# Performance work log

Hardware: AMD Instinct MI355X
Metric: run time of the kernel (lower is better)

## Reference

```python
import jax, jax.numpy as jnp
import numpy as np
from jax import lax

PAD, EOS, SOS = 0, 1, 2
B, S, V, NT, E, H = 64, 256, 50000, 64, 300, 500  # H = hidden per direction (HIDDEN_SIZE//2)


def setup_inputs():
    key = jax.random.key(0)
    ks = jax.random.split(key, 24)
    x = jax.random.randint(ks[0], (B, S), 1, V)          # no PAD tokens -> mask all ones
    y0 = jax.random.randint(ks[1], (B, S), 3, NT)        # gold tags, avoid special tags
    embed = jax.random.normal(ks[2], (V, E)) * 0.1
    embed = embed.at[PAD].set(0.0)                       # padding_idx=PAD
    inp = {"x": x, "y0": y0, "embed": embed}
    ki = 3
    for l, din in enumerate([E, 2 * H]):                 # layer0 in=E, layer1 in=2H
        for d in ("f", "b"):
            inp[f"w_ih_l{l}{d}"] = jax.random.normal(ks[ki], (4 * H, din)) * 0.05; ki += 1
            inp[f"w_hh_l{l}{d}"] = jax.random.normal(ks[ki], (4 * H, H)) * 0.05; ki += 1
            inp[f"b_l{l}{d}"] = jnp.zeros((4 * H,))       # b_ih + b_hh combined
    inp["W_out"] = jax.random.normal(ks[ki], (NT, 2 * H)) * 0.05; ki += 1
    inp["b_out"] = jnp.zeros((NT,))
    trans = jax.random.normal(ks[ki], (NT, NT))
    trans = trans.at[SOS, :].set(-10000.0).at[:, EOS].set(-10000.0)
    trans = trans.at[:, PAD].set(-10000.0).at[PAD, :].set(-10000.0)
    trans = trans.at[PAD, EOS].set(0.0).at[PAD, PAD].set(0.0)
    inp["trans"] = trans
    return inp


def _lstm_dir(xs, w_ih, w_hh, b, reverse):
    # xs: [B,S,D] -> outputs [B,S,H]; PyTorch gate order i,f,g,o
    def step(carry, x_t):
        h, c = carry
        g = x_t @ w_ih.T + h @ w_hh.T + b
        i, f, gg, o = jnp.split(g, 4, axis=-1)
        c = jax.nn.sigmoid(f) * c + jax.nn.sigmoid(i) * jnp.tanh(gg)
        h = jax.nn.sigmoid(o) * jnp.tanh(c)
        return (h, c), h
    bz = xs.shape[0]
    init = (jnp.zeros((bz, H), xs.dtype), jnp.zeros((bz, H), xs.dtype))
    _, hs = lax.scan(step, init, jnp.swapaxes(xs, 0, 1), reverse=reverse)
    return jnp.swapaxes(hs, 0, 1)


def _forward(x, y0, embed, w_ih_l0f, w_hh_l0f, b_l0f, w_ih_l0b, w_hh_l0b, b_l0b,
             w_ih_l1f, w_hh_l1f, b_l1f, w_ih_l1b, w_hh_l1b, b_l1b, W_out, b_out, trans):
    h0 = embed[x]                                        # [B,S,E]
    h1 = jnp.concatenate([_lstm_dir(h0, w_ih_l0f, w_hh_l0f, b_l0f, False),
                          _lstm_dir(h0, w_ih_l0b, w_hh_l0b, b_l0b, True)], -1)
    h2 = jnp.concatenate([_lstm_dir(h1, w_ih_l1f, w_hh_l1f, b_l1f, False),
                          _lstm_dir(h1, w_ih_l1b, w_hh_l1b, b_l1b, True)], -1)
    mask = (x > 0).astype(h2.dtype)                      # [B,S]
    emit = (h2 @ W_out.T + b_out) * mask[..., None]      # [B,S,NT]
    # --- CRF partition function Z (batched logsumexp DP) ---
    score0 = jnp.full((B, NT), -10000.0, emit.dtype).at[:, SOS].set(0.0)
    def step(score, inp):
        e_t, m_t = inp                                   # [B,NT], [B]
        # new[b,i] = lse_j(score[b,j] + trans[i,j] + e_t[b,i])
        z = score[:, None, :] + trans[None, :, :] + e_t[:, :, None]
        new = jax.nn.logsumexp(z, axis=-1)
        return jnp.where(m_t[:, None] > 0, new, score), None
    scoreZ, _ = lax.scan(step, score0, (jnp.swapaxes(emit, 0, 1), jnp.swapaxes(mask, 0, 1)))
    Z = jax.nn.logsumexp(scoreZ, axis=-1)                # [B]
    # --- gold path score ---
    yext = jnp.concatenate([jnp.full((B, 1), SOS, dtype=y0.dtype), y0], 1)  # [B,S+1]
    e_gold = jnp.take_along_axis(emit, yext[:, 1:, None], axis=-1)[..., 0]   # [B,S]
    t_gold = trans[yext[:, 1:], yext[:, :-1]] * mask                         # [B,S]
    gold = jnp.sum(e_gold + t_gold, axis=1)
    return Z - gold                                      # [B] NLL per sample


def reference(x, y0, embed, w_ih_l0f, w_hh_l0f, b_l0f, w_ih_l0b, w_hh_l0b, b_l0b,
              w_ih_l1f, w_hh_l1f, b_l1f, w_ih_l1b, w_hh_l1b, b_l1b, W_out, b_out, trans):
    return _forward(x, y0, embed, w_ih_l0f, w_hh_l0f, b_l0f, w_ih_l0b, w_hh_l0b, b_l0b,
                    w_ih_l1f, w_hh_l1f, b_l1f, w_ih_l1b, w_hh_l1b, b_l1b, W_out, b_out, trans)
```

## Files before the change

### kernel.cpp

```cpp
#include <hip/hip_runtime.h>
#include <hip/hip_bf16.h>
#include <cstdint>

#define B_ 64
#define S_ 256
#define V_ 50000
#define NT_ 64
#define E_ 300
#define H_ 500
#define SOS_ 2

typedef __hip_bfloat16 bf16;
typedef unsigned short ushort_t;
typedef __attribute__((ext_vector_type(8))) __bf16 v8bf;
typedef __attribute__((ext_vector_type(4))) float f32x4;
typedef __attribute__((ext_vector_type(4))) unsigned int u32x4;

__device__ __forceinline__ float sigm(float x) { return 1.f / (1.f + __expf(-x)); }
__device__ __forceinline__ float tanh_fast(float x) {
    float xx = fminf(fmaxf(x, -15.f), 15.f);
    float e = __expf(2.f * xx);
    return (e - 1.f) / (e + 1.f);
}

__device__ __forceinline__ float bfu_to_f(ushort_t u) {
    unsigned int v = ((unsigned int)u) << 16;
    return __builtin_bit_cast(float, v);
}
__device__ __forceinline__ ushort_t f_to_bfu(float f) {
    return __builtin_bit_cast(ushort_t, __float2bfloat16(f));
}

__device__ __forceinline__ void store_val(float* p, float v) { *p = v; }
__device__ __forceinline__ void store_val(ushort_t* p, float v) { *p = f_to_bfu(v); }

__device__ __forceinline__ v8bf load16_coh(const ushort_t* p) {
    v8bf r;
    asm volatile("global_load_dwordx4 %0, %1, off sc0 sc1" : "=v"(r) : "v"(p) : "memory");
    return r;
}
__device__ __forceinline__ void store8_coh(ushort_t* p, uint2 v) {
    asm volatile("global_store_dwordx2 %0, %1, off sc0 sc1" :: "v"(p), "v"(v) : "memory");
}

__global__ void dbg_kernel(float* out, float v) {
    if (threadIdx.x < 64) out[threadIdx.x] = v;
}

__global__ void gather_kernel(const int* __restrict__ x, const float* __restrict__ embed,
                              ushort_t* __restrict__ h0) {
    int m = blockIdx.x;
    int tok = x[m];
    const float* src = embed + (size_t)tok * E_;
    ushort_t* dst = h0 + (size_t)m * 320;
    for (int e = threadIdx.x; e < 320; e += blockDim.x)
        dst[e] = (e < E_) ? f_to_bfu(src[e]) : (ushort_t)0;
}

__global__ void conv_w_kernel(const float* __restrict__ in, ushort_t* __restrict__ out,
                              int N, int Kout, int Kin, int split, int real) {
    int idx = blockIdx.x * 256 + threadIdx.x;
    if (idx >= N * Kout) return;
    int n = idx / Kout, k = idx % Kout;
    int half = (k >= split) ? 1 : 0;
    int ki = k - half * split;
    float v = (ki < real) ? in[(size_t)n * Kin + half * real + ki] : 0.f;
    out[idx] = f_to_bfu(v);
}

template <bool HS>
__device__ __forceinline__ float loadA(const ushort_t* A, int m, int k, int K) {
    size_t idx;
    if (HS) {
        int dir = (k >= H_) ? 1 : 0;
        idx = (((size_t)dir * B_ + (m >> 8)) * S_ + (m & 255)) * 512 + (k - dir * H_);
    } else {
        idx = (size_t)m * K + k;
    }
    return bfu_to_f(A[idx]);
}

template <bool HS, typename OutT>
__global__ __launch_bounds__(256) void gemm_nt(const ushort_t* __restrict__ A,
                                               const float* __restrict__ W0,
                                               const float* __restrict__ b0,
                                               OutT* __restrict__ C0,
                                               int M, int N, int K) {
    const float* W = W0;
    const float* bias = b0;
    OutT* C = C0;
    const int n0 = blockIdx.y * 64;
    const int tid = threadIdx.x;
    const int tx = tid & 15, ty = tid >> 4;

    __shared__ float As[16][68];
    __shared__ float Bs[16][68];

    float acc[4][4] = {};

    for (int k0 = 0; k0 < K; k0 += 16) {
        for (int e = tid; e < 1024; e += 256) {
            int r = e >> 4, kk = e & 15;
            int k = k0 + kk;
            int m = blockIdx.x * 64 + r;
            As[kk][r] = (k < K) ? loadA<HS>(A, m, k, K) : 0.f;
            int n = n0 + r;
            Bs[kk][r] = (k < K && n < N) ? W[(size_t)n * K + k] : 0.f;
        }
        __syncthreads();
#pragma unroll
        for (int kk = 0; kk < 16; ++kk) {
            float4 a = *(const float4*)&As[kk][ty << 2];
            float4 w = *(const float4*)&Bs[kk][tx << 2];
            acc[0][0] += a.x * w.x; acc[0][1] += a.x * w.y; acc[0][2] += a.x * w.z; acc[0][3] += a.x * w.w;
            acc[1][0] += a.y * w.x; acc[1][1] += a.y * w.y; acc[1][2] += a.y * w.z; acc[1][3] += a.y * w.w;
            acc[2][0] += a.z * w.x; acc[2][1] += a.z * w.y; acc[2][2] += a.z * w.z; acc[2][3] += a.z * w.w;
            acc[3][0] += a.w * w.x; acc[3][1] += a.w * w.y; acc[3][2] += a.w * w.z; acc[3][3] += a.w * w.w;
        }
        __syncthreads();
    }

#pragma unroll
    for (int i = 0; i < 4; ++i) {
        int r = (ty << 2) + i;
        int m = blockIdx.x * 64 + r;
#pragma unroll
        for (int j = 0; j < 4; ++j) {
            int n = n0 + (tx << 2) + j;
            if (n < N) store_val(&C[(size_t)m * N + n], acc[i][j] + bias[n]);
        }
    }
}

template <int AV>
__global__ __launch_bounds__(256) void gemm_mfma(const ushort_t* __restrict__ A,
                                                 const ushort_t* __restrict__ Wf,
                                                 const ushort_t* __restrict__ Wb,
                                                 const float* __restrict__ bf_,
                                                 const float* __restrict__ bb_,
                                                 ushort_t* __restrict__ Cf,
                                                 ushort_t* __restrict__ Cb,
                                                 int Nn, int Kp) {
    const ushort_t* W = blockIdx.z ? Wb : Wf;
    const float* bias = blockIdx.z ? bb_ : bf_;
    ushort_t* C = blockIdx.z ? Cb : Cf;
    const int t = blockIdx.x;
    const int n0 = blockIdx.y * 64;
    const int tid = threadIdx.x;
    const int lane = tid & 63;
    const int wv = tid >> 6;
    const int wn = wv & 1, wb = wv >> 1;
    const int l15 = lane & 15, kgrp = lane >> 4;

    __shared__ ushort_t wlds[64 * 64];

    f32x4 acc[2][2] = {};

    for (int k0 = 0; k0 < Kp; k0 += 64) {
        if (k0) __syncthreads();
#pragma unroll
        for (int c = 0; c < 2; ++c) {
            int ch = tid + c * 256;
            int rrow = ch >> 3, kc = ch & 7;
            int n = n0 + rrow, k = k0 + kc * 8;
            v8bf wv8;
            if (n < Nn) {
                wv8 = *(const v8bf*)(W + (size_t)n * Kp + k);
            } else {
                u32x4 z = {0u, 0u, 0u, 0u};
                wv8 = __builtin_bit_cast(v8bf, z);
            }
            int off = (rrow * 128 + kc * 16) ^ ((rrow & 7) << 4);
            *(v8bf*)((char*)wlds + off) = wv8;
        }
        __syncthreads();

#pragma unroll
        for (int ks = 0; ks < 2; ++ks) {
            int kk = k0 + ks * 32 + kgrp * 8;
            int br0 = wb * 32 + l15;
            const ushort_t* pb0;
            const ushort_t* pb1;
            if (AV == 0) {
                pb0 = A + ((size_t)(br0 * 256 + t)) * 320 + kk;
                pb1 = A + ((size_t)((br0 + 16) * 256 + t)) * 320 + kk;
            } else {
                int dir = kk >> 9, kr = kk & 511;
                pb0 = A + (((size_t)(dir * B_ + br0) * S_) + t) * 512 + kr;
                pb1 = A + (((size_t)(dir * B_ + br0 + 16) * S_) + t) * 512 + kr;
            }
            v8bf b0v = *(const v8bf*)pb0;
            v8bf b1v = *(const v8bf*)pb1;
            int r0 = wn * 32 + l15;
            int aoff0 = (r0 * 128 + ks * 64 + kgrp * 16) ^ ((r0 & 7) << 4);
            int aoff1 = ((r0 + 16) * 128 + ks * 64 + kgrp * 16) ^ ((r0 & 7) << 4);
            v8bf a0 = *(const v8bf*)((const char*)wlds + aoff0);
            v8bf a1 = *(const v8bf*)((const char*)wlds + aoff1);
            acc[0][0] = __builtin_amdgcn_mfma_f32_16x16x32_bf16(a0, b0v, acc[0][0], 0, 0, 0);
            acc[0][1] = __builtin_amdgcn_mfma_f32_16x16x32_bf16(a0, b1v, acc[0][1], 0, 0, 0);
            acc[1][0] = __builtin_amdgcn_mfma_f32_16x16x32_bf16(a1, b0v, acc[1][0], 0, 0, 0);
            acc[1][1] = __builtin_amdgcn_mfma_f32_16x16x32_bf16(a1, b1v, acc[1][1], 0, 0, 0);
        }
    }

#pragma unroll
    for (int nsub = 0; nsub < 2; ++nsub) {
#pragma unroll
        for (int bsub = 0; bsub < 2; ++bsub) {
#pragma unroll
            for (int r = 0; r < 4; ++r) {
                int n = n0 + wn * 32 + nsub * 16 + kgrp * 4 + r;
                if (n < Nn) {
                    int bcol = wb * 32 + bsub * 16 + l15;
                    C[(((size_t)t * 4 + (bcol >> 4)) * Nn + n) * 16 + (bcol & 15)] =
                        f_to_bfu(acc[nsub][bsub][r] + bias[n]);
                }
            }
        }
    }
}

__global__ __launch_bounds__(128, 1) void lstm_wave_kernel(
        const ushort_t* __restrict__ Gf, const ushort_t* __restrict__ Gb,
        const float* __restrict__ Whh_f, const float* __restrict__ Whh_b,
        ushort_t* __restrict__ hseq,
        int* __restrict__ flags) {
    const int bid = blockIdx.x;
    const int dir = bid >> 7;
    const int shard = (bid >> 2) & 31;
    const int bgrp = bid & 3;
    const int tid = threadIdx.x;
    const int w = tid >> 6;
    const int lane = tid & 63;
    const int l15 = lane & 15, kgrp = lane >> 4;
    const int batch = bgrp * 16 + l15;
    const int n0c = shard * 16;
    const int domain = dir * 4 + bgrp;

    const ushort_t* G = dir ? Gb : Gf;
    const float* Whh = dir ? Whh_b : Whh_f;

    __shared__ float xlds[2][16][64];

    v8bf wreg[4][8];
    {
        int g = l15 & 3;
        int colbase = n0c + (l15 >> 2) * 4;
#pragma unroll
        for (int j = 0; j < 4; ++j) {
            int col = colbase + j;
            bool cok = col < H_;
            const float* wrow = Whh + ((size_t)g * H_ + (cok ? col : 0)) * H_;
#pragma unroll
            for (int ki = 0; ki < 8; ++ki) {
                union { ushort_t u[8]; v8bf v; } tmp;
#pragma unroll
                for (int e = 0; e < 8; ++e) {
                    int k = w * 256 + ki * 32 + kgrp * 8 + e;
                    tmp.u[e] = (cok && k < H_) ? f_to_bfu(wrow[k]) : (ushort_t)0;
                }
                wreg[j][ki] = tmp.v;
            }
        }
    }

    float c[4] = {0.f, 0.f, 0.f, 0.f};

    for (int s = 0; s < S_; ++s) {
        const int tr = dir ? (S_ - 1 - s) : s;

        float p[4][4];
        if (w == 0) {
#pragma unroll
            for (int j = 0; j < 4; ++j) {
                int col = n0c + kgrp * 4 + j;
                int colc = (col < H_) ? col : (H_ - 1);
#pragma unroll
                for (int g = 0; g < 4; ++g)
                    p[j][g] = bfu_to_f(G[(((size_t)tr * 4 + bgrp) * 2000 + g * H_ + colc) * 16 + l15]);
            }
        }
        asm volatile("" ::: "memory");

        f32x4 acc[4] = {};
        if (s > 0) {
            {
                const int need = s;
                int fi = domain * 32 + w * 16 + (lane & 15);
                while (true) {
                    int f = (lane < 16)
                        ? __hip_atomic_load(&flags[fi], __ATOMIC_RELAXED, __HIP_MEMORY_SCOPE_AGENT)
                        : need;
                    if (__all(f >= need)) break;
                    __builtin_amdgcn_s_sleep(1);
                }
            }
            asm volatile("" ::: "memory");

            const int trp = dir ? (tr + 1) : (tr - 1);
            const ushort_t* hrow = hseq + (((size_t)dir * B_ + batch) * S_ + trp) * 512 + w * 256;
            v8bf bfr[8];
#pragma unroll
            for (int ki = 0; ki < 8; ++ki)
                bfr[ki] = load16_coh(hrow + ki * 32 + kgrp * 8);
            asm volatile("s_waitcnt vmcnt(0)" ::: "memory");
            __builtin_amdgcn_sched_barrier(0);

#pragma unroll
            for (int ki = 0; ki < 8; ++ki)
#pragma unroll
                for (int j = 0; j < 4; ++j)
                    acc[j] = __builtin_amdgcn_mfma_f32_16x16x32_bf16(wreg[j][ki], bfr[ki], acc[j], 0, 0, 0);
        }

        if (w == 1) {
#pragma unroll
            for (int j = 0; j < 4; ++j)
#pragma unroll
                for (int r = 0; r < 4; ++r)
                    xlds[s & 1][j * 4 + r][lane] = acc[j][r];
        }
        __syncthreads();

        if (w == 0) {
            ushort_t hv[4];
#pragma unroll
            for (int j = 0; j < 4; ++j) {
                float gi = p[j][0] + acc[j][0] + xlds[s & 1][j * 4 + 0][lane];
                float gf = p[j][1] + acc[j][1] + xlds[s & 1][j * 4 + 1][lane];
                float gg = p[j][2] + acc[j][2] + xlds[s & 1][j * 4 + 2][lane];
                float go = p[j][3] + acc[j][3] + xlds[s & 1][j * 4 + 3][lane];
                c[j] = sigm(gf) * c[j] + sigm(gi) * tanh_fast(gg);
                hv[j] = f_to_bfu(sigm(go) * tanh_fast(c[j]));
            }
            int colb = n0c + kgrp * 4;
            if (colb < H_) {
                uint2 pk;
                pk.x = (unsigned)hv[0] | ((unsigned)hv[1] << 16);
                pk.y = (unsigned)hv[2] | ((unsigned)hv[3] << 16);
                store8_coh(hseq + (((size_t)dir * B_ + batch) * S_ + tr) * 512 + colb, pk);
            }
            asm volatile("s_waitcnt vmcnt(0)" ::: "memory");
            if (lane == 0)
                __hip_atomic_store(&flags[domain * 32 + shard], s + 1,
                                   __ATOMIC_RELAXED, __HIP_MEMORY_SCOPE_AGENT);
        }
    }
}

__global__ __launch_bounds__(256) void crf_kernel(const float* __restrict__ emit,
                                                  const float* __restrict__ trans,
                                                  const int* __restrict__ x,
                                                  const int* __restrict__ y0,
                                                  float* __restrict__ out) {
    const int b = blockIdx.x, tid = threadIdx.x;
    __shared__ float tr[64][65];
    __shared__ float sc[2][64];
    __shared__ float zsh;
    __shared__ float red[4];

    for (int e = tid; e < 4096; e += 256) tr[e >> 6][e & 63] = trans[e];
    if (tid < 64) sc[0][tid] = (tid == SOS_) ? 0.f : -10000.f;
    __syncthreads();

    const int i = tid >> 2, sub = tid & 3;
    int cur = 0;
    for (int t = 0; t < S_; ++t) {
        int m = x[b * S_ + t] > 0;
        float v[16];
        float vmax = -3.0e38f;
#pragma unroll
        for (int jj = 0; jj < 16; ++jj) {
            int j = (sub << 4) + jj;
            v[jj] = sc[cur][j] + tr[i][j];
            vmax = fmaxf(vmax, v[jj]);
        }
        vmax = fmaxf(vmax, __shfl_xor(vmax, 1, 64));
        vmax = fmaxf(vmax, __shfl_xor(vmax, 2, 64));
        float s = 0.f;
#pragma unroll
        for (int jj = 0; jj < 16; ++jj) s += __expf(v[jj] - vmax);
        s += __shfl_xor(s, 1, 64);
        s += __shfl_xor(s, 2, 64);
        float lse = vmax + __logf(s);
        float e_i = emit[((size_t)b * S_ + t) * NT_ + i];
        if (sub == 0) sc[cur ^ 1][i] = m ? (lse + e_i) : sc[cur][i];
        __syncthreads();
        cur ^= 1;
    }

    if (tid < 64) {
        float v2 = sc[cur][tid];
        float mz = v2;
        for (int d = 1; d < 64; d <<= 1) mz = fmaxf(mz, __shfl_xor(mz, d, 64));
        float sz = __expf(v2 - mz);
        for (int d = 1; d < 64; d <<= 1) sz += __shfl_xor(sz, d, 64);
        if (tid == 0) zsh = mz + __logf(sz);
    }
    __syncthreads();

    {
        int t = tid;
        int m = x[b * S_ + t] > 0;
        int yc = y0[b * S_ + t];
        int yp = t ? y0[b * S_ + t - 1] : SOS_;
        float term = m ? (emit[((size_t)b * S_ + t) * NT_ + yc] + tr[yc][yp]) : 0.f;
        for (int d = 1; d < 64; d <<= 1) term += __shfl_xor(term, d, 64);
        if ((tid & 63) == 0) red[tid >> 6] = term;
    }
    __syncthreads();
    if (tid == 0) out[b] = zsh - (red[0] + red[1] + red[2] + red[3]);
}

extern "C" void kernel_launch(void* const* d_in, const int* in_sizes, int n_in,
                              void* d_out, int out_size, void* d_ws, size_t ws_size,
                              hipStream_t stream) {
    const int* x = (const int*)d_in[0];
    const int* y0 = (const int*)d_in[1];
    const float* embed = (const float*)d_in[2];
    const float* w_ih_l0f = (const float*)d_in[3];
    const float* w_hh_l0f = (const float*)d_in[4];
    const float* b_l0f = (const float*)d_in[5];
    const float* w_ih_l0b = (const float*)d_in[6];
    const float* w_hh_l0b = (const float*)d_in[7];
    const float* b_l0b = (const float*)d_in[8];
    const float* w_ih_l1f = (const float*)d_in[9];
    const float* w_hh_l1f = (const float*)d_in[10];
    const float* b_l1f = (const float*)d_in[11];
    const float* w_ih_l1b = (const float*)d_in[12];
    const float* w_hh_l1b = (const float*)d_in[13];
    const float* b_l1b = (const float*)d_in[14];
    const float* W_out = (const float*)d_in[15];
    const float* b_out = (const float*)d_in[16];
    const float* trans = (const float*)d_in[17];
    float* outp = (float*)d_out;

    char* ws = (char*)d_ws;
    size_t off = 0;
    auto alloc = [&](size_t bytes) {
        void* p = ws + off;
        off += (bytes + 255) & ~(size_t)255;
        return p;
    };
    ushort_t* h0 = (ushort_t*)alloc((size_t)B_ * S_ * 320 * 2);
    ushort_t* hseq = (ushort_t*)alloc((size_t)2 * B_ * S_ * 512 * 2);
    float* emitb = (float*)alloc((size_t)B_ * S_ * NT_ * 4);
    ushort_t* Gf = (ushort_t*)alloc((size_t)S_ * 2000 * 64 * 2);
    ushort_t* Gb = (ushort_t*)alloc((size_t)S_ * 2000 * 64 * 2);
    int* flags = (int*)alloc((size_t)2 * 8 * 32 * 4);
    (void)in_sizes; (void)n_in; (void)out_size;

    ushort_t* Wl0f = (ushort_t*)emitb;
    ushort_t* Wl0b = Wl0f + (size_t)2000 * 320;
    ushort_t* Wl1f = (ushort_t*)h0;
    ushort_t* Wl1b = Wl1f + (size_t)2000 * 1024;

    if (off > ws_size) {
        dbg_kernel<<<1, 64, 0, stream>>>(outp, (float)(ws_size / 1048576.0));
        return;
    }

    const int M = B_ * S_;

    hipMemsetAsync(flags, 0, (size_t)2 * 8 * 32 * 4, stream);
    hipMemsetAsync(hseq, 0, (size_t)2 * B_ * S_ * 512 * 2, stream);

    gather_kernel<<<M, 128, 0, stream>>>(x, embed, h0);

    {
        int tot = 2000 * 320, nb = (tot + 255) / 256;
        conv_w_kernel<<<nb, 256, 0, stream>>>(w_ih_l0f, Wl0f, 2000, 320, 300, 320, 300);
        conv_w_kernel<<<nb, 256, 0, stream>>>(w_ih_l0b, Wl0b, 2000, 320, 300, 320, 300);
    }

    gemm_mfma<0><<<dim3(S_, 32, 2), 256, 0, stream>>>(
        h0, Wl0f, Wl0b, b_l0f, b_l0b, Gf, Gb, 2000, 320);

    {
        int tot = 2000 * 1024, nb = (tot + 255) / 256;
        conv_w_kernel<<<nb, 256, 0, stream>>>(w_ih_l1f, Wl1f, 2000, 1024, 1000, 512, 500);
        conv_w_kernel<<<nb, 256, 0, stream>>>(w_ih_l1b, Wl1b, 2000, 1024, 1000, 512, 500);
    }

    lstm_wave_kernel<<<256, 128, 0, stream>>>(Gf, Gb, w_hh_l0f, w_hh_l0b, hseq, flags);

    gemm_mfma<1><<<dim3(S_, 32, 2), 256, 0, stream>>>(
        hseq, Wl1f, Wl1b, b_l1f, b_l1b, Gf, Gb, 2000, 1024);

    lstm_wave_kernel<<<256, 128, 0, stream>>>(Gf, Gb, w_hh_l1f, w_hh_l1b, hseq, flags + 256);

    gemm_nt<true, float><<<dim3(M / 64, 1, 1), 256, 0, stream>>>(
        hseq, W_out, b_out, emitb, M, NT_, 2 * H_);

    crf_kernel<<<B_, 256, 0, stream>>>(emitb, trans, x, y0, outp);
}
```

Baseline: 2.859 ms.

## Replace LSTM flag handshake with sentinel-polled hidden state and prefetch GEMM weight tiles

The cross-block flag-based synchronisation in the persistent LSTM kernel is removed. Consumers now poll the hidden-state buffer itself, which is pre-filled with an all-ones NaN sentinel, until no sentinel dwords remain. This drops a waitcnt, an atomic store and a separate flag poll from each timestep's critical path. The cost is an extra full-buffer init kernel before each layer. Correctness now depends on 8-byte stores being observed atomically and on real bf16 pairs never equalling 0xFFFFFFFF. Separately, the input GEMM register-prefetches the next weight tile while computing on the current one.

```diff
diff --git a/kernel.cpp b/kernel.cpp
--- a/kernel.cpp
+++ b/kernel.cpp
@@ -45,6 +45,11 @@
 
 __global__ void dbg_kernel(float* out, float v) {
     if (threadIdx.x < 64) out[threadIdx.x] = v;
+}
+
+__global__ void init_hseq_kernel(unsigned int* __restrict__ hseq_dw) {
+    unsigned int* p = hseq_dw + (size_t)blockIdx.x * 256;
+    p[threadIdx.x] = (threadIdx.x < 250) ? 0xFFFFFFFFu : 0u;
 }
 
 __global__ void gather_kernel(const int* __restrict__ x, const float* __restrict__ embed,
@@ -154,26 +159,37 @@
 
     __shared__ ushort_t wlds[64 * 64];
 
+    const int rrow = tid >> 3, kc = tid & 7;
+    const int rrow2 = (tid + 256) >> 3;
+
+    auto load_tile = [&](int k0, v8bf* nxt) {
+#pragma unroll
+        for (int c = 0; c < 2; ++c) {
+            int rr = c ? rrow2 : rrow;
+            int n = n0 + rr, k = k0 + kc * 8;
+            if (n < Nn) {
+                nxt[c] = *(const v8bf*)(W + (size_t)n * Kp + k);
+            } else {
+                u32x4 z = {0u, 0u, 0u, 0u};
+                nxt[c] = __builtin_bit_cast(v8bf, z);
+            }
+        }
+    };
+
     f32x4 acc[2][2] = {};
+    v8bf nxt[2];
+    load_tile(0, nxt);
 
     for (int k0 = 0; k0 < Kp; k0 += 64) {
         if (k0) __syncthreads();
 #pragma unroll
         for (int c = 0; c < 2; ++c) {
-            int ch = tid + c * 256;
-            int rrow = ch >> 3, kc = ch & 7;
-            int n = n0 + rrow, k = k0 + kc * 8;
-            v8bf wv8;
-            if (n < Nn) {
-                wv8 = *(const v8bf*)(W + (size_t)n * Kp + k);
-            } else {
-                u32x4 z = {0u, 0u, 0u, 0u};
-                wv8 = __builtin_bit_cast(v8bf, z);
-            }
-            int off = (rrow * 128 + kc * 16) ^ ((rrow & 7) << 4);
-            *(v8bf*)((char*)wlds + off) = wv8;
+            int rr = c ? rrow2 : rrow;
+            int off = (rr * 128 + kc * 16) ^ ((rr & 7) << 4);
+            *(v8bf*)((char*)wlds + off) = nxt[c];
         }
         __syncthreads();
+        if (k0 + 64 < Kp) load_tile(k0 + 64, nxt);
 
 #pragma unroll
         for (int ks = 0; ks < 2; ++ks) {
@@ -223,8 +239,7 @@
 __global__ __launch_bounds__(128, 1) void lstm_wave_kernel(
         const ushort_t* __restrict__ Gf, const ushort_t* __restrict__ Gb,
         const float* __restrict__ Whh_f, const float* __restrict__ Whh_b,
-        ushort_t* __restrict__ hseq,
-        int* __restrict__ flags) {
+        ushort_t* __restrict__ hseq) {
     const int bid = blockIdx.x;
     const int dir = bid >> 7;
     const int shard = (bid >> 2) & 31;
@@ -235,7 +250,6 @@
     const int l15 = lane & 15, kgrp = lane >> 4;
     const int batch = bgrp * 16 + l15;
     const int n0c = shard * 16;
-    const int domain = dir * 4 + bgrp;
 
     const ushort_t* G = dir ? Gb : Gf;
     const float* Whh = dir ? Whh_b : Whh_f;
@@ -284,26 +298,28 @@
 
         f32x4 acc[4] = {};
         if (s > 0) {
-            {
-                const int need = s;
-                int fi = domain * 32 + w * 16 + (lane & 15);
-                while (true) {
-                    int f = (lane < 16)
-                        ? __hip_atomic_load(&flags[fi], __ATOMIC_RELAXED, __HIP_MEMORY_SCOPE_AGENT)
-                        : need;
-                    if (__all(f >= need)) break;
-                    __builtin_amdgcn_s_sleep(1);
-                }
-            }
-            asm volatile("" ::: "memory");
-
             const int trp = dir ? (tr + 1) : (tr - 1);
             const ushort_t* hrow = hseq + (((size_t)dir * B_ + batch) * S_ + trp) * 512 + w * 256;
             v8bf bfr[8];
 #pragma unroll
             for (int ki = 0; ki < 8; ++ki)
                 bfr[ki] = load16_coh(hrow + ki * 32 + kgrp * 8);
-            asm volatile("s_waitcnt vmcnt(0)" ::: "memory");
+            while (true) {
+                asm volatile("s_waitcnt vmcnt(0)" ::: "memory");
+                __builtin_amdgcn_sched_barrier(0);
+                unsigned bad = 0u;
+#pragma unroll
+                for (int ki = 0; ki < 8; ++ki) {
+                    u32x4 dw = __builtin_bit_cast(u32x4, bfr[ki]);
+#pragma unroll
+                    for (int d = 0; d < 4; ++d)
+                        bad |= (dw[d] == 0xFFFFFFFFu) ? 1u : 0u;
+                }
+                if (!__any((int)bad)) break;
+#pragma unroll
+                for (int ki = 0; ki < 8; ++ki)
+                    bfr[ki] = load16_coh(hrow + ki * 32 + kgrp * 8);
+            }
             __builtin_amdgcn_sched_barrier(0);
 
 #pragma unroll
@@ -340,10 +356,6 @@
                 pk.y = (unsigned)hv[2] | ((unsigned)hv[3] << 16);
                 store8_coh(hseq + (((size_t)dir * B_ + batch) * S_ + tr) * 512 + colb, pk);
             }
-            asm volatile("s_waitcnt vmcnt(0)" ::: "memory");
-            if (lane == 0)
-                __hip_atomic_store(&flags[domain * 32 + shard], s + 1,
-                                   __ATOMIC_RELAXED, __HIP_MEMORY_SCOPE_AGENT);
         }
     }
 }
@@ -447,7 +459,6 @@
     float* emitb = (float*)alloc((size_t)B_ * S_ * NT_ * 4);
     ushort_t* Gf = (ushort_t*)alloc((size_t)S_ * 2000 * 64 * 2);
     ushort_t* Gb = (ushort_t*)alloc((size_t)S_ * 2000 * 64 * 2);
-    int* flags = (int*)alloc((size_t)2 * 8 * 32 * 4);
     (void)in_sizes; (void)n_in; (void)out_size;
 
     ushort_t* Wl0f = (ushort_t*)emitb;
@@ -462,8 +473,7 @@
 
     const int M = B_ * S_;
 
-    hipMemsetAsync(flags, 0, (size_t)2 * 8 * 32 * 4, stream);
-    hipMemsetAsync(hseq, 0, (size_t)2 * B_ * S_ * 512 * 2, stream);
+    init_hseq_kernel<<<2 * B_ * S_, 256, 0, stream>>>((unsigned int*)hseq);
 
     gather_kernel<<<M, 128, 0, stream>>>(x, embed, h0);
 
@@ -482,12 +492,14 @@
         conv_w_kernel<<<nb, 256, 0, stream>>>(w_ih_l1b, Wl1b, 2000, 1024, 1000, 512, 500);
     }
 
-    lstm_wave_kernel<<<256, 128, 0, stream>>>(Gf, Gb, w_hh_l0f, w_hh_l0b, hseq, flags);
+    lstm_wave_kernel<<<256, 128, 0, stream>>>(Gf, Gb, w_hh_l0f, w_hh_l0b, hseq);
 
     gemm_mfma<1><<<dim3(S_, 32, 2), 256, 0, stream>>>(
         hseq, Wl1f, Wl1b, b_l1f, b_l1b, Gf, Gb, 2000, 1024);
 
-    lstm_wave_kernel<<<256, 128, 0, stream>>>(Gf, Gb, w_hh_l1f, w_hh_l1b, hseq, flags + 256);
+    init_hseq_kernel<<<2 * B_ * S_, 256, 0, stream>>>((unsigned int*)hseq);
+
+    lstm_wave_kernel<<<256, 128, 0, stream>>>(Gf, Gb, w_hh_l1f, w_hh_l1b, hseq);
 
     gemm_nt<true, float><<<dim3(M / 64, 1, 1), 256, 0, stream>>>(
         hseq, W_out, b_out, emitb, M, NT_, 2 * H_);
```

After: 3.640 ms. 27.3% more time.
